# Performance work log

Measured on AMD Instinct MI355X. Metric: run time of the kernel, lower is better.

## Reference

```python
import jax, jax.numpy as jnp
import numpy as np
from jax import lax

DN = ('NCDHW', 'OIDHW', 'NCDHW')
EPS = 1e-5  # torch BatchNorm1d default eps


def _cexp(v):
    # broadcast a per-channel vector over NCDHW
    return v[None, :, None, None, None]


def _bn_relu(y, g, b, rm, rv):
    inv = g * lax.rsqrt(rv + EPS)
    return jax.nn.relu((y - _cexp(rm)) * _cexp(inv) + _cexp(b))


def setup_inputs() -> dict:
    key = jax.random.key(0)
    ks = jax.random.split(key, 18)
    B, D = 2, 65
    C1, C2, CO = 1, 32, 100
    mask0 = (jax.random.uniform(ks[0], (B, 1, D, D, D)) < 0.1).astype(jnp.int32)
    x = jax.random.normal(ks[1], (B, C1, D, D, D), jnp.float32) * mask0.astype(jnp.float32)

    def w(k, shape, fan):
        return jax.random.normal(k, shape, jnp.float32) * np.float32(1.0 / np.sqrt(fan))

    return {
        'x': x, 'mask0': mask0,
        'W1': w(ks[2], (C2, C1, 3, 3, 3), C1 * 27), 'b1': w(ks[3], (C2,), C2),
        'g1': jax.random.uniform(ks[4], (C2,), jnp.float32, 0.5, 1.5),
        'bt1': w(ks[5], (C2,), C2),
        'rm1': 0.1 * jax.random.normal(ks[6], (C2,), jnp.float32),
        'rv1': jax.random.uniform(ks[7], (C2,), jnp.float32, 0.5, 1.5),
        'W2': w(ks[8], (C2, C2, 3, 3, 3), C2 * 27), 'b2': w(ks[9], (C2,), C2),
        'g2': jax.random.uniform(ks[10], (C2,), jnp.float32, 0.5, 1.5),
        'bt2': w(ks[11], (C2,), C2),
        'rm2': 0.1 * jax.random.normal(ks[12], (C2,), jnp.float32),
        'rv2': jax.random.uniform(ks[13], (C2,), jnp.float32, 0.5, 1.5),
        'Winv': w(ks[14], (CO, C2, 3, 3, 3), C2 * 27), 'binv': w(ks[15], (CO,), CO),
    }


def reference(x, mask0, W1, b1, g1, bt1, rm1, rv1,
              W2, b2, g2, bt2, rm2, rv2, Winv, binv):
    m0 = mask0.astype(x.dtype)  # [B,1,D,D,D] active input sites
    # --- SparseConv3d(1,32,k=3,s=2): dense conv is exact on zero-padded sparse features
    y1 = lax.conv_general_dilated(x, W1, (2, 2, 2), 'VALID', dimension_numbers=DN) + _cexp(b1)
    # output-active sites: any active voxel in the 3^3 receptive field
    ones_k = jnp.ones((1, 1, 3, 3, 3), x.dtype)
    cnt = lax.conv_general_dilated(m0, ones_k, (2, 2, 2), 'VALID', dimension_numbers=DN)
    m1 = (cnt > 0).astype(x.dtype)  # [B,1,Do,Do,Do]
    h1 = _bn_relu(y1, g1, bt1, rm1, rv1) * m1  # BN(eval)+ReLU only on active sites
    # --- SubMConv3d(32,32,k=3): same resolution, outputs only at active sites m1
    y2 = lax.conv_general_dilated(h1, W2, (1, 1, 1), [(1, 1)] * 3, dimension_numbers=DN) + _cexp(b2)
    h2 = _bn_relu(y2, g2, bt2, rm2, rv2) * m1
    # --- SparseInverseConv3d(32,100,k=3, indice_key='conv1'): transposed-rulebook scatter
    # back to the original conv1 input sites == stride-2 transposed conv masked by m0.
    y3 = lax.conv_general_dilated(h2, Winv, (1, 1, 1), [(2, 2)] * 3,
                                  lhs_dilation=(2, 2, 2), dimension_numbers=DN)
    out = (y3 + _cexp(binv)) * m0  # features exist only at original active voxels
    return out
```

## Files before the change

### kernel.cpp

```cpp
#include <hip/hip_runtime.h>

#define BATCH 2
#define DIN 65
#define D2IN (65*65)
#define D3IN (65*65*65)
#define NTOT (2*D3IN)
#define DO 32
#define DP 34
#define C2 32
#define CO 100
#define CAP 8192
#define EPS 1e-5f

typedef __attribute__((ext_vector_type(8))) short short8;
typedef __attribute__((ext_vector_type(4))) float floatx4;

#define H1B_OFF 0
#define H2B_OFF 1257728
#define M1_OFF  2515456
#define WB2_OFF 2580992
#define WB3_OFF 2594816
#define CNT8_OFF 2643200
#define VOX_OFF 2643208
#define SIDX_OFF 2708744
#define RES_OFF 3258000

__device__ __forceinline__ unsigned short f2bf(float f) {
    unsigned int u = __float_as_uint(f);
    return (unsigned short)((u + 0x7fffu + ((u >> 16) & 1u)) >> 16);
}

__global__ __launch_bounds__(256) void kprep(
    uint4* __restrict__ zp, int n4,
    const float* __restrict__ W2, const float* __restrict__ Winv,
    unsigned short* __restrict__ wb2, unsigned short* __restrict__ wb3,
    int* __restrict__ cnt8)
{
    int gid = blockIdx.x * 256 + threadIdx.x;
    int stride = gridDim.x * 256;
    uint4 zv; zv.x = 0; zv.y = 0; zv.z = 0; zv.w = 0;
    for (int i = gid; i < n4; i += stride) zp[i] = zv;

    for (int q = gid; q < 27 * 2 * 64; q += stride) {
        int tap = q >> 7, r = q & 127, ct = r >> 6, lane = r & 63;
        int n = ct * 16 + (lane & 15), kq = lane >> 4;
        union { unsigned short h[8]; uint4 v; } u;
#pragma unroll
        for (int j = 0; j < 8; j++) {
            int k = kq * 8 + j;
            u.h[j] = f2bf(W2[n * 864 + k * 27 + tap]);
        }
        *(uint4*)(wb2 + q * 8) = u.v;
    }
    for (int q = gid; q < 27 * 7 * 64; q += stride) {
        int tap = q / 448, r = q % 448, ct = r >> 6, lane = r & 63;
        int co = ct * 16 + (lane & 15), kq = lane >> 4;
        union { unsigned short h[8]; uint4 v; } u;
#pragma unroll
        for (int j = 0; j < 8; j++) {
            int k = kq * 8 + j;
            u.h[j] = (co < 100) ? f2bf(Winv[(co * 32 + k) * 27 + tap]) : (unsigned short)0;
        }
        *(uint4*)(wb3 + q * 8) = u.v;
    }
    if (gid < 8) cnt8[gid] = 0;
}

__global__ __launch_bounds__(256) void kcompact(
    const int* __restrict__ mask0, int* __restrict__ sidx,
    int* __restrict__ vox, int* __restrict__ cnt8)
{
    __shared__ int lcnt[8], lbase[8];
    int tid = threadIdx.x;
    const int chunk = (NTOT + 255) / 256;
    int start = blockIdx.x * chunk;
    int end = start + chunk; if (end > NTOT) end = NTOT;
    if (tid < 8) lcnt[tid] = 0;
    __syncthreads();
    for (int t = start + tid; t < end; t += 256) {
        if (mask0[t]) {
            int r = t % D3IN;
            int z = r / D2IN; int rem = r % D2IN;
            int y = rem / DIN; int x = rem % DIN;
            atomicAdd(&lcnt[((z & 1) << 2) | ((y & 1) << 1) | (x & 1)], 1);
        }
    }
    __syncthreads();
    if (tid < 8) {
        lbase[tid] = lcnt[tid] ? atomicAdd(&cnt8[tid], lcnt[tid]) : 0;
        lcnt[tid] = 0;
    }
    __syncthreads();
    for (int t = start + tid; t < end; t += 256) {
        int s = -1;
        if (mask0[t]) {
            int bb = t / D3IN; int r = t % D3IN;
            int z = r / D2IN; int rem = r % D2IN;
            int y = rem / DIN; int x = rem % DIN;
            int cls = ((z & 1) << 2) | ((y & 1) << 1) | (x & 1);
            int loff = atomicAdd(&lcnt[cls], 1);
            int slot = lbase[cls] + loff;
            if (slot < CAP) {
                s = cls * CAP + slot;
                vox[s] = (bb << 21) | (z << 14) | (y << 7) | x;
            }
        }
        sidx[t] = s;
    }
}

__global__ __launch_bounds__(128) void k1(
    const float* __restrict__ x, const int* __restrict__ mask0,
    const float* __restrict__ W1, const float* __restrict__ b1,
    const float* __restrict__ g1, const float* __restrict__ bt1,
    const float* __restrict__ rm1, const float* __restrict__ rv1,
    unsigned short* __restrict__ h1b, float* __restrict__ m1)
{
    int t = blockIdx.x * 128 + threadIdx.x;
    int b = t >> 15, r = t & 32767;
    int z = r >> 10, y = (r >> 5) & 31, xo = r & 31;

    const float* xb = x + b * D3IN;
    const int*   mb = mask0 + b * D3IN;

    float xv[27];
    int any = 0;
#pragma unroll
    for (int kd = 0; kd < 3; kd++)
#pragma unroll
        for (int kh = 0; kh < 3; kh++)
#pragma unroll
            for (int kw = 0; kw < 3; kw++) {
                int idx = (2 * z + kd) * D2IN + (2 * y + kh) * DIN + (2 * xo + kw);
                xv[kd * 9 + kh * 3 + kw] = xb[idx];
                any |= mb[idx];
            }
    float m1f = any ? 1.0f : 0.0f;
    m1[t] = m1f;

    union { unsigned short h[32]; uint4 v[4]; } u;
#pragma unroll 4
    for (int co = 0; co < 32; co++) {
        float a = 0.f;
#pragma unroll
        for (int k = 0; k < 27; k++) a += xv[k] * W1[co * 27 + k];
        float s = g1[co] * rsqrtf(rv1[co] + EPS);
        float v = (a + b1[co] - rm1[co]) * s + bt1[co];
        u.h[co] = f2bf(fmaxf(v, 0.f) * m1f);
    }
    uint4* out4 = (uint4*)(h1b + (size_t)((((b * DP + z + 1) * DP + (y + 1)) * DP + (xo + 1)) * C2));
#pragma unroll
    for (int q = 0; q < 4; q++) out4[q] = u.v[q];
}

__global__ __launch_bounds__(256) void k2(
    const unsigned short* __restrict__ h1b, const unsigned short* __restrict__ wb2,
    const float* __restrict__ b2, const float* __restrict__ g2,
    const float* __restrict__ bt2, const float* __restrict__ rm2,
    const float* __restrict__ rv2, const float* __restrict__ m1,
    unsigned short* __restrict__ h2b)
{
    int tid = threadIdx.x;
    int wv = tid >> 6, lane = tid & 63;
    int mtile = blockIdx.x * 4 + wv;
    int v0 = mtile * 16;
    int b = v0 >> 15, r = v0 & 32767;
    int z = r >> 10, y = (r >> 5) & 31, x0 = r & 31;

    int m = lane & 15, kq = lane >> 4;
    const unsigned short* abase = h1b +
        (size_t)((((b * DP + z) * DP + y) * DP + x0 + m) * C2 + kq * 8);

    floatx4 acc[2];
    acc[0] = (floatx4){0.f, 0.f, 0.f, 0.f};
    acc[1] = (floatx4){0.f, 0.f, 0.f, 0.f};

    for (int kd = 0; kd < 3; kd++)
#pragma unroll
        for (int kh = 0; kh < 3; kh++)
#pragma unroll
            for (int kw = 0; kw < 3; kw++) {
                int tap = (kd * 3 + kh) * 3 + kw;
                short8 a = *(const short8*)(abase + ((kd * DP + kh) * DP + kw) * C2);
                short8 w0 = *(const short8*)(wb2 + ((tap * 2 + 0) * 64 + lane) * 8);
                short8 w1 = *(const short8*)(wb2 + ((tap * 2 + 1) * 64 + lane) * 8);
                acc[0] = __builtin_amdgcn_mfma_f32_16x16x32_bf16(a, w0, acc[0], 0, 0, 0);
                acc[1] = __builtin_amdgcn_mfma_f32_16x16x32_bf16(a, w1, acc[1], 0, 0, 0);
            }

    float mf[4];
#pragma unroll
    for (int i = 0; i < 4; i++) mf[i] = m1[v0 + kq * 4 + i];
#pragma unroll
    for (int ct = 0; ct < 2; ct++) {
        int co = ct * 16 + m;
        float s = g2[co] * rsqrtf(rv2[co] + EPS);
        float sh = (b2[co] - rm2[co]) * s + bt2[co];
#pragma unroll
        for (int i = 0; i < 4; i++) {
            int row = kq * 4 + i;
            float val = fmaxf(acc[ct][i] * s + sh, 0.f) * mf[i];
            h2b[(size_t)((((b * DP + z + 1) * DP + (y + 1)) * DP + (x0 + row + 1)) * C2 + co)]
                = f2bf(val);
        }
    }
}

__global__ __launch_bounds__(256) void k3compute(
    const unsigned short* __restrict__ h2b, const unsigned short* __restrict__ wb3,
    const float* __restrict__ binv, const int* __restrict__ vox,
    const int* __restrict__ cnt8, float* __restrict__ res)
{
    int cls = blockIdx.y;
    int pd = (cls >> 2) & 1, ph = (cls >> 1) & 1, pw = cls & 1;
    int nh = 2 - ph, nw = 2 - pw, nhw = nh * nw;
    int ntap = (2 - pd) * nhw;
    int tid = threadIdx.x;
    int wv = tid >> 6, lane = tid & 63;
    int m = lane & 15, kq = lane >> 4;

    int n = cnt8[cls]; if (n > CAP) n = CAP;
    int ntiles = (n + 15) >> 4;

    float bv[7];
#pragma unroll
    for (int ct = 0; ct < 7; ct++) {
        int co = ct * 16 + m;
        bv[ct] = (co < 100) ? binv[co] : 0.f;
    }

    for (int t = blockIdx.x * 4 + wv; t < ntiles; t += 64 * 4) {
        int idx = t * 16 + m; if (idx >= n) idx = n - 1;
        unsigned int pv = (unsigned int)vox[cls * CAP + idx];
        int xx = pv & 127, yy = (pv >> 7) & 127, zz = (pv >> 14) & 127, bb = (pv >> 21) & 1;
        const unsigned short* abase = h2b +
            (size_t)(((((bb * DP + (zz >> 1) + pd) * DP + (yy >> 1) + ph) * DP
                       + (xx >> 1) + pw)) * C2 + kq * 8);

        floatx4 acc[7];
#pragma unroll
        for (int ct = 0; ct < 7; ct++) acc[ct] = (floatx4){0.f, 0.f, 0.f, 0.f};

        for (int tl = 0; tl < ntap; tl++) {
            int td = tl / nhw, rr = tl % nhw, th = rr / nw, tw = rr % nw;
            int tap = (pd + 2 * td) * 9 + (ph + 2 * th) * 3 + (pw + 2 * tw);
            short8 a = *(const short8*)(abase + ((td * DP + th) * DP + tw) * C2);
#pragma unroll
            for (int ct = 0; ct < 7; ct++) {
                short8 w = *(const short8*)(wb3 + ((tap * 7 + ct) * 64 + lane) * 8);
                acc[ct] = __builtin_amdgcn_mfma_f32_16x16x32_bf16(a, w, acc[ct], 0, 0, 0);
            }
        }
#pragma unroll
        for (int ct = 0; ct < 7; ct++) {
            int co = ct * 16 + m;
#pragma unroll
            for (int i = 0; i < 4; i++) {
                int ridx = t * 16 + kq * 4 + i;
                if (ridx < n)
                    res[(size_t)(cls * CAP + ridx) * 112 + co] = acc[ct][i] + bv[ct];
            }
        }
    }
}

__global__ __launch_bounds__(256) void k3write(
    const float* __restrict__ res, const int* __restrict__ sidx,
    float* __restrict__ out)
{
    __shared__ int ls[65];
    int blk = blockIdx.x;
    int y = blk % 65; int t2 = blk / 65;
    int z = t2 % 65;  int b = t2 / 65;
    int tid = threadIdx.x;
    int roff = b * D3IN + z * D2IN + y * DIN;
    if (tid < 65) ls[tid] = sidx[roff + tid];
    __syncthreads();

    int wv = tid >> 6, lane = tid & 63;
    int s = ls[lane];
    int s64 = ls[64];
    float* obase = out + (size_t)b * 100 * D3IN + z * D2IN + y * DIN;

#pragma unroll 5
    for (int j = 0; j < 25; j++) {
        int co = wv * 25 + j;
        float val = (s >= 0) ? res[(size_t)s * 112 + co] : 0.f;
        float* orow = obase + (size_t)co * D3IN;
        orow[lane] = val;
        if (lane == 0)
            orow[64] = (s64 >= 0) ? res[(size_t)s64 * 112 + co] : 0.f;
    }
}

extern "C" void kernel_launch(void* const* d_in, const int* in_sizes, int n_in,
                              void* d_out, int out_size, void* d_ws, size_t ws_size,
                              hipStream_t stream) {
    const float* x    = (const float*)d_in[0];
    const int*  mask0 = (const int*)  d_in[1];
    const float* W1   = (const float*)d_in[2];
    const float* b1   = (const float*)d_in[3];
    const float* g1   = (const float*)d_in[4];
    const float* bt1  = (const float*)d_in[5];
    const float* rm1  = (const float*)d_in[6];
    const float* rv1  = (const float*)d_in[7];
    const float* W2   = (const float*)d_in[8];
    const float* b2   = (const float*)d_in[9];
    const float* g2   = (const float*)d_in[10];
    const float* bt2  = (const float*)d_in[11];
    const float* rm2  = (const float*)d_in[12];
    const float* rv2  = (const float*)d_in[13];
    const float* Winv = (const float*)d_in[14];
    const float* binv = (const float*)d_in[15];

    float* ws = (float*)d_ws;
    unsigned short* h1b = (unsigned short*)(ws + H1B_OFF);
    unsigned short* h2b = (unsigned short*)(ws + H2B_OFF);
    float* m1   = ws + M1_OFF;
    unsigned short* wb2 = (unsigned short*)(ws + WB2_OFF);
    unsigned short* wb3 = (unsigned short*)(ws + WB3_OFF);
    int*   cnt8 = (int*)(ws + CNT8_OFF);
    int*   vox  = (int*)(ws + VOX_OFF);
    int*   sidx = (int*)(ws + SIDX_OFF);
    float* res  = ws + RES_OFF;

    int n4 = (2 * 2515456) / 8;
    kprep<<<1024, 256, 0, stream>>>((uint4*)ws, n4, W2, Winv, wb2, wb3, cnt8);

    kcompact<<<256, 256, 0, stream>>>(mask0, sidx, vox, cnt8);

    k1<<<512, 128, 0, stream>>>(x, mask0, W1, b1, g1, bt1, rm1, rv1, h1b, m1);

    k2<<<1024, 256, 0, stream>>>(h1b, wb2, b2, g2, bt2, rm2, rv2, m1, h2b);

    k3compute<<<dim3(64, 8), 256, 0, stream>>>(h2b, wb3, binv, vox, cnt8, res);

    k3write<<<2 * 65 * 65, 256, 0, stream>>>(res, sidx, (float*)d_out);
}
```

Measured before the change: 369.1 us.

## Merge prep, compaction and conv1 into one launch; zero only halos; vectorize scatter reads

```diff
diff --git a/kernel.cpp b/kernel.cpp
--- a/kernel.cpp
+++ b/kernel.cpp
@@ -20,7 +20,7 @@
 #define M1_OFF  2515456
 #define WB2_OFF 2580992
 #define WB3_OFF 2594816
-#define CNT8_OFF 2643200
+#define CNT8_OFF (2643200)
 #define VOX_OFF 2643208
 #define SIDX_OFF 2708744
 #define RES_OFF 3258000
@@ -30,127 +30,133 @@
     return (unsigned short)((u + 0x7fffu + ((u >> 16) & 1u)) >> 16);
 }
 
-__global__ __launch_bounds__(256) void kprep(
-    uint4* __restrict__ zp, int n4,
-    const float* __restrict__ W2, const float* __restrict__ Winv,
-    unsigned short* __restrict__ wb2, unsigned short* __restrict__ wb3,
-    int* __restrict__ cnt8)
-{
-    int gid = blockIdx.x * 256 + threadIdx.x;
-    int stride = gridDim.x * 256;
-    uint4 zv; zv.x = 0; zv.y = 0; zv.z = 0; zv.w = 0;
-    for (int i = gid; i < n4; i += stride) zp[i] = zv;
-
-    for (int q = gid; q < 27 * 2 * 64; q += stride) {
-        int tap = q >> 7, r = q & 127, ct = r >> 6, lane = r & 63;
-        int n = ct * 16 + (lane & 15), kq = lane >> 4;
-        union { unsigned short h[8]; uint4 v; } u;
-#pragma unroll
-        for (int j = 0; j < 8; j++) {
-            int k = kq * 8 + j;
-            u.h[j] = f2bf(W2[n * 864 + k * 27 + tap]);
-        }
-        *(uint4*)(wb2 + q * 8) = u.v;
-    }
-    for (int q = gid; q < 27 * 7 * 64; q += stride) {
-        int tap = q / 448, r = q % 448, ct = r >> 6, lane = r & 63;
-        int co = ct * 16 + (lane & 15), kq = lane >> 4;
-        union { unsigned short h[8]; uint4 v; } u;
-#pragma unroll
-        for (int j = 0; j < 8; j++) {
-            int k = kq * 8 + j;
-            u.h[j] = (co < 100) ? f2bf(Winv[(co * 32 + k) * 27 + tap]) : (unsigned short)0;
-        }
-        *(uint4*)(wb3 + q * 8) = u.v;
-    }
-    if (gid < 8) cnt8[gid] = 0;
-}
-
-__global__ __launch_bounds__(256) void kcompact(
-    const int* __restrict__ mask0, int* __restrict__ sidx,
-    int* __restrict__ vox, int* __restrict__ cnt8)
-{
-    __shared__ int lcnt[8], lbase[8];
-    int tid = threadIdx.x;
-    const int chunk = (NTOT + 255) / 256;
-    int start = blockIdx.x * chunk;
-    int end = start + chunk; if (end > NTOT) end = NTOT;
-    if (tid < 8) lcnt[tid] = 0;
-    __syncthreads();
-    for (int t = start + tid; t < end; t += 256) {
-        if (mask0[t]) {
-            int r = t % D3IN;
-            int z = r / D2IN; int rem = r % D2IN;
-            int y = rem / DIN; int x = rem % DIN;
-            atomicAdd(&lcnt[((z & 1) << 2) | ((y & 1) << 1) | (x & 1)], 1);
-        }
-    }
-    __syncthreads();
-    if (tid < 8) {
-        lbase[tid] = lcnt[tid] ? atomicAdd(&cnt8[tid], lcnt[tid]) : 0;
-        lcnt[tid] = 0;
-    }
-    __syncthreads();
-    for (int t = start + tid; t < end; t += 256) {
-        int s = -1;
-        if (mask0[t]) {
-            int bb = t / D3IN; int r = t % D3IN;
-            int z = r / D2IN; int rem = r % D2IN;
-            int y = rem / DIN; int x = rem % DIN;
-            int cls = ((z & 1) << 2) | ((y & 1) << 1) | (x & 1);
-            int loff = atomicAdd(&lcnt[cls], 1);
-            int slot = lbase[cls] + loff;
-            if (slot < CAP) {
-                s = cls * CAP + slot;
-                vox[s] = (bb << 21) | (z << 14) | (y << 7) | x;
-            }
-        }
-        sidx[t] = s;
-    }
-}
-
-__global__ __launch_bounds__(128) void k1(
+__global__ __launch_bounds__(256) void f1(
     const float* __restrict__ x, const int* __restrict__ mask0,
     const float* __restrict__ W1, const float* __restrict__ b1,
     const float* __restrict__ g1, const float* __restrict__ bt1,
     const float* __restrict__ rm1, const float* __restrict__ rv1,
-    unsigned short* __restrict__ h1b, float* __restrict__ m1)
+    const float* __restrict__ W2, const float* __restrict__ Winv,
+    unsigned short* __restrict__ h1b, unsigned short* __restrict__ h2b,
+    float* __restrict__ m1,
+    unsigned short* __restrict__ wb2, unsigned short* __restrict__ wb3,
+    int* __restrict__ sidx, int* __restrict__ vox, int* __restrict__ cnt8)
 {
-    int t = blockIdx.x * 128 + threadIdx.x;
-    int b = t >> 15, r = t & 32767;
-    int z = r >> 10, y = (r >> 5) & 31, xo = r & 31;
-
-    const float* xb = x + b * D3IN;
-    const int*   mb = mask0 + b * D3IN;
-
-    float xv[27];
-    int any = 0;
-#pragma unroll
-    for (int kd = 0; kd < 3; kd++)
-#pragma unroll
-        for (int kh = 0; kh < 3; kh++)
-#pragma unroll
-            for (int kw = 0; kw < 3; kw++) {
-                int idx = (2 * z + kd) * D2IN + (2 * y + kh) * DIN + (2 * xo + kw);
-                xv[kd * 9 + kh * 3 + kw] = xb[idx];
-                any |= mb[idx];
-            }
-    float m1f = any ? 1.0f : 0.0f;
-    m1[t] = m1f;
-
-    union { unsigned short h[32]; uint4 v[4]; } u;
+    __shared__ int lcnt[8], lbase[8];
+    int bid = blockIdx.x, tid = threadIdx.x;
+
+    if (bid < 256) {
+        const int chunk = (NTOT + 255) / 256;
+        int start = bid * chunk;
+        int end = start + chunk; if (end > NTOT) end = NTOT;
+        if (tid < 8) lcnt[tid] = 0;
+        __syncthreads();
+        for (int t = start + tid; t < end; t += 256) {
+            if (mask0[t]) {
+                int r = t % D3IN;
+                int z = r / D2IN; int rem = r % D2IN;
+                int y = rem / DIN; int xx = rem % DIN;
+                atomicAdd(&lcnt[((z & 1) << 2) | ((y & 1) << 1) | (xx & 1)], 1);
+            }
+        }
+        __syncthreads();
+        if (tid < 8) {
+            lbase[tid] = lcnt[tid] ? atomicAdd(&cnt8[tid], lcnt[tid]) : 0;
+            lcnt[tid] = 0;
+        }
+        __syncthreads();
+        for (int t = start + tid; t < end; t += 256) {
+            int s = -1;
+            if (mask0[t]) {
+                int bb = t / D3IN; int r = t % D3IN;
+                int z = r / D2IN; int rem = r % D2IN;
+                int y = rem / DIN; int xx = rem % DIN;
+                int cls = ((z & 1) << 2) | ((y & 1) << 1) | (xx & 1);
+                int loff = atomicAdd(&lcnt[cls], 1);
+                int slot = lbase[cls] + loff;
+                if (slot < CAP) {
+                    s = cls * CAP + slot;
+                    vox[s] = (bb << 21) | (z << 14) | (y << 7) | xx;
+                }
+            }
+            sidx[t] = s;
+        }
+    } else if (bid < 512) {
+        int t = (bid - 256) * 256 + tid;
+        int b = t >> 15, r = t & 32767;
+        int z = r >> 10, y = (r >> 5) & 31, xo = r & 31;
+
+        const float* xb = x + b * D3IN;
+        const int*   mb = mask0 + b * D3IN;
+
+        float xv[27];
+        int any = 0;
+#pragma unroll
+        for (int kd = 0; kd < 3; kd++)
+#pragma unroll
+            for (int kh = 0; kh < 3; kh++)
+#pragma unroll
+                for (int kw = 0; kw < 3; kw++) {
+                    int idx = (2 * z + kd) * D2IN + (2 * y + kh) * DIN + (2 * xo + kw);
+                    xv[kd * 9 + kh * 3 + kw] = xb[idx];
+                    any |= mb[idx];
+                }
+        float m1f = any ? 1.0f : 0.0f;
+        m1[t] = m1f;
+
+        union { unsigned short h[32]; uint4 v[4]; } u;
 #pragma unroll 4
-    for (int co = 0; co < 32; co++) {
-        float a = 0.f;
-#pragma unroll
-        for (int k = 0; k < 27; k++) a += xv[k] * W1[co * 27 + k];
-        float s = g1[co] * rsqrtf(rv1[co] + EPS);
-        float v = (a + b1[co] - rm1[co]) * s + bt1[co];
-        u.h[co] = f2bf(fmaxf(v, 0.f) * m1f);
-    }
-    uint4* out4 = (uint4*)(h1b + (size_t)((((b * DP + z + 1) * DP + (y + 1)) * DP + (xo + 1)) * C2));
-#pragma unroll
-    for (int q = 0; q < 4; q++) out4[q] = u.v[q];
+        for (int co = 0; co < 32; co++) {
+            float a = 0.f;
+#pragma unroll
+            for (int k = 0; k < 27; k++) a += xv[k] * W1[co * 27 + k];
+            float s = g1[co] * rsqrtf(rv1[co] + EPS);
+            float v = (a + b1[co] - rm1[co]) * s + bt1[co];
+            u.h[co] = f2bf(fmaxf(v, 0.f) * m1f);
+        }
+        uint4* out4 = (uint4*)(h1b + (size_t)((((b * DP + z + 1) * DP + (y + 1)) * DP + (xo + 1)) * C2));
+#pragma unroll
+        for (int q = 0; q < 4; q++) out4[q] = u.v[q];
+    } else if (bid < 820) {
+        int gid = (bid - 512) * 256 + tid;
+        if (gid < 2 * 39304) {
+            int b = gid / 39304; int r = gid % 39304;
+            int z = r / 1156; int rem = r % 1156;
+            int y = rem / 34; int xx = rem % 34;
+            if (z == 0 || z == 33 || y == 0 || y == 33 || xx == 0 || xx == 33) {
+                size_t off = (size_t)((((b * DP + z) * DP + y) * DP + xx) * C2);
+                uint4 zv; zv.x = 0; zv.y = 0; zv.z = 0; zv.w = 0;
+                uint4* p1 = (uint4*)(h1b + off);
+                uint4* p2 = (uint4*)(h2b + off);
+#pragma unroll
+                for (int q = 0; q < 4; q++) { p1[q] = zv; p2[q] = zv; }
+            }
+        }
+    } else {
+        int gid = (bid - 820) * 256 + tid;
+        if (gid < 27 * 2 * 64) {
+            int q = gid;
+            int tap = q >> 7, r = q & 127, ct = r >> 6, lane = r & 63;
+            int n = ct * 16 + (lane & 15), kq = lane >> 4;
+            union { unsigned short h[8]; uint4 v; } u;
+#pragma unroll
+            for (int j = 0; j < 8; j++) {
+                int k = kq * 8 + j;
+                u.h[j] = f2bf(W2[n * 864 + k * 27 + tap]);
+            }
+            *(uint4*)(wb2 + q * 8) = u.v;
+        } else if (gid < 27 * 2 * 64 + 27 * 7 * 64) {
+            int q = gid - 27 * 2 * 64;
+            int tap = q / 448, r = q % 448, ct = r >> 6, lane = r & 63;
+            int co = ct * 16 + (lane & 15), kq = lane >> 4;
+            union { unsigned short h[8]; uint4 v; } u;
+#pragma unroll
+            for (int j = 0; j < 8; j++) {
+                int k = kq * 8 + j;
+                u.h[j] = (co < 100) ? f2bf(Winv[(co * 32 + k) * 27 + tap]) : (unsigned short)0;
+            }
+            *(uint4*)(wb3 + q * 8) = u.v;
+        }
+    }
 }
 
 __global__ __launch_bounds__(256) void k2(
@@ -280,16 +286,37 @@
     int wv = tid >> 6, lane = tid & 63;
     int s = ls[lane];
     int s64 = ls[64];
+
+    union { float4 q[7]; float f[28]; } u;
+    if (s >= 0) {
+        const float4* rp = (const float4*)(res + (size_t)s * 112 + wv * 28);
+#pragma unroll
+        for (int j = 0; j < 7; j++) u.q[j] = rp[j];
+    } else {
+#pragma unroll
+        for (int j = 0; j < 7; j++) u.q[j] = make_float4(0.f, 0.f, 0.f, 0.f);
+    }
+    union { float4 q[7]; float f[28]; } u64;
+    if (lane == 0) {
+        if (s64 >= 0) {
+            const float4* rp = (const float4*)(res + (size_t)s64 * 112 + wv * 28);
+#pragma unroll
+            for (int j = 0; j < 7; j++) u64.q[j] = rp[j];
+        } else {
+#pragma unroll
+            for (int j = 0; j < 7; j++) u64.q[j] = make_float4(0.f, 0.f, 0.f, 0.f);
+        }
+    }
+
     float* obase = out + (size_t)b * 100 * D3IN + z * D2IN + y * DIN;
-
-#pragma unroll 5
-    for (int j = 0; j < 25; j++) {
-        int co = wv * 25 + j;
-        float val = (s >= 0) ? res[(size_t)s * 112 + co] : 0.f;
-        float* orow = obase + (size_t)co * D3IN;
-        orow[lane] = val;
-        if (lane == 0)
-            orow[64] = (s64 >= 0) ? res[(size_t)s64 * 112 + co] : 0.f;
+#pragma unroll
+    for (int j = 0; j < 28; j++) {
+        int co = wv * 28 + j;
+        if (co < 100) {
+            float* orow = obase + (size_t)co * D3IN;
+            orow[lane] = u.f[j];
+            if (lane == 0) orow[64] = u64.f[j];
+        }
     }
 }
 
@@ -324,12 +351,10 @@
     int*   sidx = (int*)(ws + SIDX_OFF);
     float* res  = ws + RES_OFF;
 
-    int n4 = (2 * 2515456) / 8;
-    kprep<<<1024, 256, 0, stream>>>((uint4*)ws, n4, W2, Winv, wb2, wb3, cnt8);
-
-    kcompact<<<256, 256, 0, stream>>>(mask0, sidx, vox, cnt8);
-
-    k1<<<512, 128, 0, stream>>>(x, mask0, W1, b1, g1, bt1, rm1, rv1, h1b, m1);
+    hipMemsetAsync(cnt8, 0, 8 * sizeof(int), stream);
+
+    f1<<<881, 256, 0, stream>>>(x, mask0, W1, b1, g1, bt1, rm1, rv1, W2, Winv,
+                                h1b, h2b, m1, wb2, wb3, sidx, vox, cnt8);
 
     k2<<<1024, 256, 0, stream>>>(h1b, wb2, b2, g2, bt2, rm2, rv2, m1, h2b);
 
```

After: 357.0 us. 3.3% less time.
